# Performance work log

Measured on AMD Instinct MI355X. Metric: run time of the kernel, lower is better.

## Reference

```python
import jax, jax.numpy as jnp
import numpy as np

B, S, D, H = 4, 2048, 1024, 16
DK = D // H

def setup_inputs() -> dict:
    key = jax.random.key(0)
    ks = jax.random.split(key, 8)
    scale = 1.0 / np.sqrt(D)
    return {
        "q": jax.random.normal(ks[0], (B, S, D), jnp.float32),
        "k": jax.random.normal(ks[1], (B, S, D), jnp.float32),
        "v": jax.random.normal(ks[2], (B, S, D), jnp.float32),
        "wq": jax.random.normal(ks[3], (D, D), jnp.float32) * scale,
        "bq": jnp.zeros((D,), jnp.float32),
        "wk": jax.random.normal(ks[4], (D, D), jnp.float32) * scale,
        "bk": jnp.zeros((D,), jnp.float32),
        "wv": jax.random.normal(ks[5], (D, D), jnp.float32) * scale,
        "bv": jnp.zeros((D,), jnp.float32),
        "wo": jax.random.normal(ks[6], (D, D), jnp.float32) * scale,
        "bo": jnp.zeros((D,), jnp.float32),
    }

def reference(q, k, v, wq, bq, wk, bk, wv, bv, wo, bo):
    b, s, _ = q.shape
    # projections; split heads -> [b, h, s, d_k]
    def proj(x, w, bias):
        y = x @ w + bias
        return y.reshape(b, -1, H, DK).transpose(0, 2, 1, 3)
    qh, kh, vh = proj(q, wq, bq), proj(k, wk, bk), proj(v, wv, bv)
    scores = jnp.einsum("bhqd,bhkd->bhqk", qh, kh) / np.sqrt(DK).astype(jnp.float32)
    attn = jax.nn.softmax(scores, axis=-1)  # dropout = identity (eval mode)
    out = jnp.einsum("bhqk,bhkd->bhqd", attn, vh)
    out = out.transpose(0, 2, 1, 3).reshape(b, s, D)
    return out @ wo + bo
```

## Files before the change

kernel.cpp:

```cpp
#include <hip/hip_runtime.h>
#include <hip/hip_bf16.h>

#define B_   4
#define S_   2048
#define D_   1024
#define H_   16
#define DK_  64
#define NTOK 8192

typedef __bf16 bf16_t;
typedef __bf16 bf16x8 __attribute__((ext_vector_type(8)));
typedef __bf16 bf16x4 __attribute__((ext_vector_type(4)));
typedef __bf16 bf16x2 __attribute__((ext_vector_type(2)));
typedef float  f32x4  __attribute__((ext_vector_type(4)));
typedef float  f32x16 __attribute__((ext_vector_type(16)));
typedef unsigned u32x4 __attribute__((ext_vector_type(4)));
typedef int    i32x2  __attribute__((ext_vector_type(2)));

__device__ __forceinline__ void gll16(const void* g, void* l) {
  __builtin_amdgcn_global_load_lds(
      (const __attribute__((address_space(1))) void*)g,
      (__attribute__((address_space(3))) void*)l,
      16, 0, 0);
}

__device__ __forceinline__ f32x4 mfma32(bf16x8 a, bf16x8 b, f32x4 c) {
  return __builtin_amdgcn_mfma_f32_16x16x32_bf16(a, b, c, 0, 0, 0);
}

__device__ __forceinline__ f32x16 mfma32x32(bf16x8 a, bf16x8 b, f32x16 c) {
#if defined(__HIP_DEVICE_COMPILE__)
  return __builtin_amdgcn_mfma_f32_32x32x16_bf16(a, b, c, 0, 0, 0);
#else
  (void)a; (void)b;
  return c;
#endif
}

__device__ __forceinline__ float fast_exp2(float x) {
#if defined(__HIP_DEVICE_COMPILE__) && __has_builtin(__builtin_amdgcn_exp2f)
  return __builtin_amdgcn_exp2f(x);
#else
  return exp2f(x);
#endif
}

__device__ __forceinline__ f32x16 zero16() {
  f32x16 z;
#pragma unroll
  for (int i = 0; i < 16; ++i) z[i] = 0.f;
  return z;
}

__device__ __forceinline__ unsigned pkbf(float lo, float hi) {
  bf16x2 t;
  t[0] = (bf16_t)lo;
  t[1] = (bf16_t)hi;
  return __builtin_bit_cast(unsigned, t);
}

__device__ __forceinline__ void plswap(unsigned &x, unsigned &y) {
#if defined(__HIP_DEVICE_COMPILE__)
  i32x2 r = __builtin_amdgcn_permlane32_swap((int)x, (int)y, false, false);
  x = (unsigned)r[0];
  y = (unsigned)r[1];
#endif
}

__device__ __forceinline__ void build_pa(const f32x16 s, bf16x8 &p0, bf16x8 &p1) {
  unsigned A0 = pkbf(fast_exp2(s[0]),  fast_exp2(s[1]));
  unsigned A1 = pkbf(fast_exp2(s[2]),  fast_exp2(s[3]));
  unsigned B0 = pkbf(fast_exp2(s[4]),  fast_exp2(s[5]));
  unsigned B1 = pkbf(fast_exp2(s[6]),  fast_exp2(s[7]));
  unsigned C0 = pkbf(fast_exp2(s[8]),  fast_exp2(s[9]));
  unsigned C1 = pkbf(fast_exp2(s[10]), fast_exp2(s[11]));
  unsigned D0 = pkbf(fast_exp2(s[12]), fast_exp2(s[13]));
  unsigned D1 = pkbf(fast_exp2(s[14]), fast_exp2(s[15]));
  plswap(A0, B0);
  plswap(A1, B1);
  plswap(C0, D0);
  plswap(C1, D1);
  u32x4 lo = {A0, A1, B0, B1};
  u32x4 hi = {C0, C1, D0, D1};
  p0 = __builtin_bit_cast(bf16x8, lo);
  p1 = __builtin_bit_cast(bf16x8, hi);
}

__global__ __launch_bounds__(256) void tobf16(
    const float* __restrict__ q, const float* __restrict__ k,
    const float* __restrict__ v, bf16_t* __restrict__ o) {
  const float* src = (blockIdx.z == 0) ? q : (blockIdx.z == 1) ? k : v;
  bf16_t* dst = o + (size_t)blockIdx.z * 8388608;
  size_t i = ((size_t)blockIdx.x * 256 + threadIdx.x) * 4;
  float4 x = *(const float4*)&src[i];
  bf16x4 y;
  y[0] = (bf16_t)x.x; y[1] = (bf16_t)x.y;
  y[2] = (bf16_t)x.z; y[3] = (bf16_t)x.w;
  *(bf16x4*)&dst[i] = y;
}

__global__ __launch_bounds__(256) void prep_weights(
    const float* __restrict__ wq, const float* __restrict__ wk,
    const float* __restrict__ wv, const float* __restrict__ wo,
    bf16_t* __restrict__ wtHi) {
  const int z = blockIdx.z;
  const float* W = (z == 0) ? wq : (z == 1) ? wk : (z == 2) ? wv : wo;
  const int k0 = blockIdx.x * 64;
  const int n0 = blockIdx.y * 64;
  const int t = threadIdx.x;
  __shared__ float T[64][65];
#pragma unroll
  for (int rr = 0; rr < 4; ++rr) {
    int row = rr * 16 + (t >> 4);
    int cc = (t & 15) * 4;
    const float4 v = *(const float4*)&W[(size_t)(k0 + row) * D_ + n0 + cc];
    T[row][cc + 0] = v.x; T[row][cc + 1] = v.y;
    T[row][cc + 2] = v.z; T[row][cc + 3] = v.w;
  }
  __syncthreads();
  const int n = t >> 2;
  const int kc = (t & 3) * 16;
  bf16x8 h0, h1;
#pragma unroll
  for (int j = 0; j < 16; ++j) {
    float vv = T[kc + j][n];
    if (j < 8) h0[j] = (bf16_t)vv;
    else       h1[j - 8] = (bf16_t)vv;
  }
  size_t ofs = (size_t)z * 1048576 + (size_t)(n0 + n) * D_ + k0 + kc;
  *(bf16x8*)&wtHi[ofs] = h0; *(bf16x8*)&wtHi[ofs + 8] = h1;
}

__global__ __launch_bounds__(256) void gemm_qkv_bf16(
    const bf16_t* __restrict__ Abf,
    const float* __restrict__ bq, const float* __restrict__ bk,
    const float* __restrict__ bv,
    const bf16_t* __restrict__ wtHi, bf16_t* __restrict__ outQKV) {
  const int z = blockIdx.z;
  const bf16_t* A   = Abf + (size_t)z * 8388608;
  const float* bias = (z == 0) ? bq : (z == 1) ? bk : bv;
  const bf16_t* WHi = wtHi + (size_t)z * 1048576;
  bf16_t* Out = outQKV + (size_t)z * 8388608;

  const int row0 = blockIdx.x * 128;
  const int col0 = blockIdx.y * 128;
  const int t = threadIdx.x;
  const int w = t >> 6, L = t & 63;
  const int m = L & 15, g = L >> 4;

  __shared__ __align__(16) bf16_t As2[128 * 64];
  __shared__ __align__(16) bf16_t Whi_s[128 * 64];

  f32x4 acc[4][4];
#pragma unroll
  for (int i = 0; i < 4; ++i)
#pragma unroll
    for (int j = 0; j < 4; ++j) acc[i][j] = (f32x4){0.f, 0.f, 0.f, 0.f};

  const int aw0 = (w & 1) * 64;
  const int bw0 = (w >> 1) * 64;

  int srow[4], scol[4];
#pragma unroll
  for (int i = 0; i < 4; ++i) {
    int slot = i * 256 + t;
    srow[i] = slot >> 3;
    scol[i] = (slot & 7) ^ (srow[i] & 7);
  }

  for (int kt = 0; kt < 16; ++kt) {
    const int k0 = kt * 64;
#pragma unroll
    for (int i = 0; i < 4; ++i) {
      gll16(&A[(size_t)(row0 + srow[i]) * D_ + k0 + scol[i] * 8],
            &As2[i * 2048 + w * 512]);
      gll16(&WHi[(size_t)(col0 + srow[i]) * D_ + k0 + scol[i] * 8],
            &Whi_s[i * 2048 + w * 512]);
    }
    __syncthreads();

#pragma unroll
    for (int kh = 0; kh < 2; ++kh) {
      bf16x8 af[4], wh[4];
#pragma unroll
      for (int it = 0; it < 4; ++it) {
        int row = aw0 + it * 16 + m;
        int sl = ((kh * 4 + g) ^ (m & 7)) * 8;
        af[it] = *(const bf16x8*)&As2[row * 64 + sl];
      }
#pragma unroll
      for (int jt = 0; jt < 4; ++jt) {
        int n = bw0 + jt * 16 + m;
        int sl = ((kh * 4 + g) ^ (m & 7)) * 8;
        wh[jt] = *(const bf16x8*)&Whi_s[n * 64 + sl];
      }
#pragma unroll
      for (int it = 0; it < 4; ++it)
#pragma unroll
        for (int jt = 0; jt < 4; ++jt)
          acc[it][jt] = mfma32(af[it], wh[jt], acc[it][jt]);
    }
    __syncthreads();
  }
#pragma unroll
  for (int jt = 0; jt < 4; ++jt) {
    int col = col0 + bw0 + jt * 16 + m;
    float bcol = bias[col];
    int h = col >> 6, d = col & 63;
#pragma unroll
    for (int it = 0; it < 4; ++it) {
      if (z != 2) {
#pragma unroll
        for (int r = 0; r < 4; ++r) {
          int row = row0 + aw0 + it * 16 + g * 4 + r;
          int b = row >> 11, s = row & 2047;
          Out[((size_t)((b * H_ + h) * S_ + s)) * DK_ + d] =
              (bf16_t)(acc[it][jt][r] + bcol);
        }
      } else {
        int row = row0 + aw0 + it * 16 + g * 4;
        int b = row >> 11, s = row & 2047;
        bf16x4 p4;
#pragma unroll
        for (int r = 0; r < 4; ++r) p4[r] = (bf16_t)(acc[it][jt][r] + bcol);
        *(bf16x4*)&Out[((size_t)((b * H_ + h) * DK_ + d)) * S_ + s] = p4;
      }
    }
  }
}

__global__ __launch_bounds__(256) void gemm_qkv_f32(
    const float* __restrict__ Aq, const float* __restrict__ Ak,
    const float* __restrict__ Av,
    const float* __restrict__ bq, const float* __restrict__ bk,
    const float* __restrict__ bv,
    const bf16_t* __restrict__ wtHi, bf16_t* __restrict__ outQKV) {
  const int z = blockIdx.z;
  const float* A    = (z == 0) ? Aq : (z == 1) ? Ak : Av;
  const float* bias = (z == 0) ? bq : (z == 1) ? bk : bv;
  const bf16_t* WHi = wtHi + (size_t)z * 1048576;
  bf16_t* Out = outQKV + (size_t)z * 8388608;

  const int row0 = blockIdx.x * 128;
  const int col0 = blockIdx.y * 128;
  const int t = threadIdx.x;
  const int w = t >> 6, L = t & 63;
  const int m = L & 15, g = L >> 4;

  __shared__ __align__(16) float  As[128 * 32];
  __shared__ __align__(16) bf16_t Whi_s[128 * 32];

  f32x4 acc[4][4];
#pragma unroll
  for (int i = 0; i < 4; ++i)
#pragma unroll
    for (int j = 0; j < 4; ++j) acc[i][j] = (f32x4){0.f, 0.f, 0.f, 0.f};

  const int aw0 = (w & 1) * 64;
  const int bw0 = (w >> 1) * 64;

  for (int kt = 0; kt < 32; ++kt) {
    const int k0 = kt * 32;
#pragma unroll
    for (int rr = 0; rr < 4; ++rr) {
      int lin16 = rr * 256 + t;
      int row = lin16 >> 3;
      int c = (lin16 & 7) ^ (row & 7);
      gll16(&A[(size_t)(row0 + row) * D_ + k0 + c * 4], &As[rr * 1024 + w * 256]);
    }
#pragma unroll
    for (int rr = 0; rr < 2; ++rr) {
      int lin16 = rr * 256 + t;
      int n = lin16 >> 2;
      int c = (lin16 & 3) ^ ((n >> 1) & 3);
      gll16(&WHi[(size_t)(col0 + n) * D_ + k0 + c * 8], &Whi_s[rr * 2048 + w * 512]);
    }
    __syncthreads();

    bf16x8 af[4], wh[4];
#pragma unroll
    for (int it = 0; it < 4; ++it) {
      int row = aw0 + it * 16 + m;
      const f32x4* p = (const f32x4*)&As[row * 32];
      f32x4 x0 = p[(2 * g) ^ (m & 7)];
      f32x4 x1 = p[(2 * g + 1) ^ (m & 7)];
      bf16x8 a;
      a[0] = (bf16_t)x0.x; a[1] = (bf16_t)x0.y; a[2] = (bf16_t)x0.z; a[3] = (bf16_t)x0.w;
      a[4] = (bf16_t)x1.x; a[5] = (bf16_t)x1.y; a[6] = (bf16_t)x1.z; a[7] = (bf16_t)x1.w;
      af[it] = a;
    }
#pragma unroll
    for (int jt = 0; jt < 4; ++jt) {
      int n = bw0 + jt * 16 + m;
      int sl = (g ^ ((m >> 1) & 3)) * 8;
      wh[jt] = *(const bf16x8*)&Whi_s[n * 32 + sl];
    }
#pragma unroll
    for (int it = 0; it < 4; ++it)
#pragma unroll
      for (int jt = 0; jt < 4; ++jt)
        acc[it][jt] = mfma32(af[it], wh[jt], acc[it][jt]);
    __syncthreads();
  }
#pragma unroll
  for (int jt = 0; jt < 4; ++jt) {
    int col = col0 + bw0 + jt * 16 + m;
    float bcol = bias[col];
    int h = col >> 6, d = col & 63;
#pragma unroll
    for (int it = 0; it < 4; ++it) {
      if (z != 2) {
#pragma unroll
        for (int r = 0; r < 4; ++r) {
          int row = row0 + aw0 + it * 16 + g * 4 + r;
          int b = row >> 11, s = row & 2047;
          Out[((size_t)((b * H_ + h) * S_ + s)) * DK_ + d] =
              (bf16_t)(acc[it][jt][r] + bcol);
        }
      } else {
        int row = row0 + aw0 + it * 16 + g * 4;
        int b = row >> 11, s = row & 2047;
        bf16x4 p4;
#pragma unroll
        for (int r = 0; r < 4; ++r) p4[r] = (bf16_t)(acc[it][jt][r] + bcol);
        *(bf16x4*)&Out[((size_t)((b * H_ + h) * DK_ + d)) * S_ + s] = p4;
      }
    }
  }
}

__global__ __launch_bounds__(256, 2) void attn(
    const bf16_t* __restrict__ Qh, const bf16_t* __restrict__ Kh,
    const bf16_t* __restrict__ VhT, bf16_t* __restrict__ Ohi) {
  const int bh = blockIdx.y;
  const int q0 = blockIdx.x * 128;
  const int t = threadIdx.x, w = t >> 6;
  const int lane = t & 63;
  const int lo5 = lane & 31, hi = lane >> 5;

  __shared__ __align__(16) bf16_t Ks[64 * 64];
  __shared__ __align__(16) bf16_t Vt[64 * 64];

  const size_t qbase = (size_t)bh * S_ * DK_;
  const size_t vbase = (size_t)bh * DK_ * S_;

  const int qrow = q0 + w * 32 + lo5;
  bf16x8 qf[4];
#pragma unroll
  for (int ks = 0; ks < 4; ++ks) {
    bf16x8 v = *(const bf16x8*)&Qh[qbase + (size_t)qrow * DK_ + ks * 16 + hi * 8];
#pragma unroll
    for (int j = 0; j < 8; ++j) v[j] = (bf16_t)(0.18033688f * (float)v[j]);
    qf[ks] = v;
  }

  bf16x8 ones;
#pragma unroll
  for (int j = 0; j < 8; ++j) ones[j] = (bf16_t)1.f;

  int offs[4];
#pragma unroll
  for (int ks = 0; ks < 4; ++ks)
    offs[ks] = lo5 * 64 + (((ks * 2 + hi) ^ (lo5 & 7)) * 8);

  f32x16 oacc0 = zero16(), oacc1 = zero16(), lacc = zero16();

  for (int kv0 = 0; kv0 < S_; kv0 += 64) {
#pragma unroll
    for (int rr = 0; rr < 2; ++rr) {
      int lin16 = rr * 256 + t;
      int rrow = lin16 >> 3;
      int c = (lin16 & 7) ^ (rrow & 7);
      gll16(&Kh[qbase + (size_t)(kv0 + rrow) * DK_ + c * 8], &Ks[rr * 2048 + w * 512]);
      gll16(&VhT[vbase + (size_t)rrow * S_ + kv0 + c * 8], &Vt[rr * 2048 + w * 512]);
    }
    __syncthreads();

    f32x16 sc0 = zero16(), sc1 = zero16();
#pragma unroll
    for (int ks = 0; ks < 4; ++ks) {
      bf16x8 k0 = *(const bf16x8*)&Ks[offs[ks]];
      bf16x8 k1 = *(const bf16x8*)&Ks[offs[ks] + 2048];
      sc0 = mfma32x32(k0, qf[ks], sc0);
      sc1 = mfma32x32(k1, qf[ks], sc1);
    }

    bf16x8 pa0, pa1, pa2, pa3;
    build_pa(sc0, pa0, pa1);
    build_pa(sc1, pa2, pa3);

#pragma unroll
    for (int ks = 0; ks < 4; ++ks) {
      bf16x8 pb = (ks == 0) ? pa0 : (ks == 1) ? pa1 : (ks == 2) ? pa2 : pa3;
      lacc = mfma32x32(ones, pb, lacc);
      bf16x8 v0 = *(const bf16x8*)&Vt[offs[ks]];
      bf16x8 v1 = *(const bf16x8*)&Vt[offs[ks] + 2048];
      oacc0 = mfma32x32(v0, pb, oacc0);
      oacc1 = mfma32x32(v1, pb, oacc1);
    }
    __syncthreads();
  }

  const int b = bh >> 4, h = bh & 15;
  const float inv = 1.f / lacc[0];
  const size_t rowofs = ((size_t)(b * S_ + qrow)) * D_ + h * DK_;
#pragma unroll
  for (int rg = 0; rg < 4; ++rg) {
    bf16x4 o0, o1;
#pragma unroll
    for (int j = 0; j < 4; ++j) {
      o0[j] = (bf16_t)(oacc0[rg * 4 + j] * inv);
      o1[j] = (bf16_t)(oacc1[rg * 4 + j] * inv);
    }
    *(bf16x4*)&Ohi[rowofs + rg * 8 + hi * 4] = o0;
    *(bf16x4*)&Ohi[rowofs + 32 + rg * 8 + hi * 4] = o1;
  }
}

__global__ __launch_bounds__(256) void gemm_out(
    const bf16_t* __restrict__ Ahi, const bf16_t* __restrict__ wtHi,
    const float* __restrict__ bias, float* __restrict__ Out) {
  const bf16_t* WHi = wtHi + (size_t)3 * 1048576;
  const int row0 = blockIdx.x * 128;
  const int col0 = blockIdx.y * 128;
  const int t = threadIdx.x;
  const int w = t >> 6, L = t & 63;
  const int m = L & 15, g = L >> 4;

  __shared__ __align__(16) bf16_t Ahi_s[128 * 64];
  __shared__ __align__(16) bf16_t Whi_s[128 * 64];

  f32x4 acc[4][4];
#pragma unroll
  for (int i = 0; i < 4; ++i)
#pragma unroll
    for (int j = 0; j < 4; ++j) acc[i][j] = (f32x4){0.f, 0.f, 0.f, 0.f};

  const int aw0 = (w & 1) * 64;
  const int bw0 = (w >> 1) * 64;

  int srow[4], scol[4];
#pragma unroll
  for (int i = 0; i < 4; ++i) {
    int slot = i * 256 + t;
    srow[i] = slot >> 3;
    scol[i] = (slot & 7) ^ (srow[i] & 7);
  }

  for (int kt = 0; kt < 16; ++kt) {
    const int k0 = kt * 64;
#pragma unroll
    for (int i = 0; i < 4; ++i) {
      gll16(&Ahi[(size_t)(row0 + srow[i]) * D_ + k0 + scol[i] * 8],
            &Ahi_s[i * 2048 + w * 512]);
      gll16(&WHi[(size_t)(col0 + srow[i]) * D_ + k0 + scol[i] * 8],
            &Whi_s[i * 2048 + w * 512]);
    }
    __syncthreads();

#pragma unroll
    for (int kh = 0; kh < 2; ++kh) {
      bf16x8 ah[4], wh[4];
#pragma unroll
      for (int it = 0; it < 4; ++it) {
        int row = aw0 + it * 16 + m;
        int sl = ((kh * 4 + g) ^ (m & 7)) * 8;
        ah[it] = *(const bf16x8*)&Ahi_s[row * 64 + sl];
      }
#pragma unroll
      for (int jt = 0; jt < 4; ++jt) {
        int n = bw0 + jt * 16 + m;
        int sl = ((kh * 4 + g) ^ (m & 7)) * 8;
        wh[jt] = *(const bf16x8*)&Whi_s[n * 64 + sl];
      }
#pragma unroll
      for (int it = 0; it < 4; ++it)
#pragma unroll
        for (int jt = 0; jt < 4; ++jt)
          acc[it][jt] = mfma32(ah[it], wh[jt], acc[it][jt]);
    }
    __syncthreads();
  }
#pragma unroll
  for (int jt = 0; jt < 4; ++jt) {
    int col = col0 + bw0 + jt * 16 + m;
    float bcol = bias[col];
#pragma unroll
    for (int it = 0; it < 4; ++it)
#pragma unroll
      for (int r = 0; r < 4; ++r) {
        int row = row0 + aw0 + it * 16 + g * 4 + r;
        Out[(size_t)row * D_ + col] = acc[it][jt][r] + bcol;
      }
  }
}

extern "C" void kernel_launch(void* const* d_in, const int* in_sizes, int n_in,
                              void* d_out, int out_size, void* d_ws, size_t ws_size,
                              hipStream_t stream) {
  const float* q  = (const float*)d_in[0];
  const float* k  = (const float*)d_in[1];
  const float* v  = (const float*)d_in[2];
  const float* wq = (const float*)d_in[3];
  const float* bq = (const float*)d_in[4];
  const float* wk = (const float*)d_in[5];
  const float* bk = (const float*)d_in[6];
  const float* wv = (const float*)d_in[7];
  const float* bv = (const float*)d_in[8];
  const float* wo = (const float*)d_in[9];
  const float* bo = (const float*)d_in[10];
  float* out = (float*)d_out;

  char* ws = (char*)d_ws;
  bf16_t* wtHi = (bf16_t*)(ws);
  bf16_t* QKVh = (bf16_t*)(ws + (8ull << 20));
  bf16_t* Ohi  = (bf16_t*)(ws + (56ull << 20));
  bf16_t* Abf  = (bf16_t*)(ws + (56ull << 20));

  const bool big = ws_size >= (104ull << 20);

  hipLaunchKernelGGL(prep_weights, dim3(16, 16, 4), dim3(256), 0, stream,
                     wq, wk, wv, wo, wtHi);
  if (big) {
    hipLaunchKernelGGL(tobf16, dim3(8192, 1, 3), dim3(256), 0, stream,
                       q, k, v, Abf);
    hipLaunchKernelGGL(gemm_qkv_bf16, dim3(64, 8, 3), dim3(256), 0, stream,
                       Abf, bq, bk, bv, wtHi, QKVh);
  } else {
    hipLaunchKernelGGL(gemm_qkv_f32, dim3(64, 8, 3), dim3(256), 0, stream,
                       q, k, v, bq, bk, bv, wtHi, QKVh);
  }
  hipLaunchKernelGGL(attn, dim3(16, 64), dim3(256), 0, stream,
                     QKVh, QKVh + 8388608, QKVh + 16777216, Ohi);
  hipLaunchKernelGGL(gemm_out, dim3(64, 8), dim3(256), 0, stream,
                     Ohi, wtHi, bo, out);
}
```

Measured before the change: 339.6 us.

## Fuse fp32-to-bf16 input conversion into QKV projection GEMM staging

Drops the separate tobf16 pass and the workspace-size branch. The QKV GEMM now loads fp32 activations into registers, packs them to bf16, and writes them into the same swizzled LDS layout the bf16 GEMM used, with 64-wide K tiles. This removes a full read-convert-write round trip of the activations through global memory and one launch. In exchange, the A-tile load becomes synchronous register loads plus LDS stores instead of async global_load_lds, which may expose load latency, and each A tile is re-read as fp32 by the 8 column blocks.

```diff
diff --git a/kernel.cpp b/kernel.cpp
--- a/kernel.cpp
+++ b/kernel.cpp
@@ -86,19 +86,6 @@
   p1 = __builtin_bit_cast(bf16x8, hi);
 }
 
-__global__ __launch_bounds__(256) void tobf16(
-    const float* __restrict__ q, const float* __restrict__ k,
-    const float* __restrict__ v, bf16_t* __restrict__ o) {
-  const float* src = (blockIdx.z == 0) ? q : (blockIdx.z == 1) ? k : v;
-  bf16_t* dst = o + (size_t)blockIdx.z * 8388608;
-  size_t i = ((size_t)blockIdx.x * 256 + threadIdx.x) * 4;
-  float4 x = *(const float4*)&src[i];
-  bf16x4 y;
-  y[0] = (bf16_t)x.x; y[1] = (bf16_t)x.y;
-  y[2] = (bf16_t)x.z; y[3] = (bf16_t)x.w;
-  *(bf16x4*)&dst[i] = y;
-}
-
 __global__ __launch_bounds__(256) void prep_weights(
     const float* __restrict__ wq, const float* __restrict__ wk,
     const float* __restrict__ wv, const float* __restrict__ wo,
@@ -131,105 +118,7 @@
   *(bf16x8*)&wtHi[ofs] = h0; *(bf16x8*)&wtHi[ofs + 8] = h1;
 }
 
-__global__ __launch_bounds__(256) void gemm_qkv_bf16(
-    const bf16_t* __restrict__ Abf,
-    const float* __restrict__ bq, const float* __restrict__ bk,
-    const float* __restrict__ bv,
-    const bf16_t* __restrict__ wtHi, bf16_t* __restrict__ outQKV) {
-  const int z = blockIdx.z;
-  const bf16_t* A   = Abf + (size_t)z * 8388608;
-  const float* bias = (z == 0) ? bq : (z == 1) ? bk : bv;
-  const bf16_t* WHi = wtHi + (size_t)z * 1048576;
-  bf16_t* Out = outQKV + (size_t)z * 8388608;
-
-  const int row0 = blockIdx.x * 128;
-  const int col0 = blockIdx.y * 128;
-  const int t = threadIdx.x;
-  const int w = t >> 6, L = t & 63;
-  const int m = L & 15, g = L >> 4;
-
-  __shared__ __align__(16) bf16_t As2[128 * 64];
-  __shared__ __align__(16) bf16_t Whi_s[128 * 64];
-
-  f32x4 acc[4][4];
-#pragma unroll
-  for (int i = 0; i < 4; ++i)
-#pragma unroll
-    for (int j = 0; j < 4; ++j) acc[i][j] = (f32x4){0.f, 0.f, 0.f, 0.f};
-
-  const int aw0 = (w & 1) * 64;
-  const int bw0 = (w >> 1) * 64;
-
-  int srow[4], scol[4];
-#pragma unroll
-  for (int i = 0; i < 4; ++i) {
-    int slot = i * 256 + t;
-    srow[i] = slot >> 3;
-    scol[i] = (slot & 7) ^ (srow[i] & 7);
-  }
-
-  for (int kt = 0; kt < 16; ++kt) {
-    const int k0 = kt * 64;
-#pragma unroll
-    for (int i = 0; i < 4; ++i) {
-      gll16(&A[(size_t)(row0 + srow[i]) * D_ + k0 + scol[i] * 8],
-            &As2[i * 2048 + w * 512]);
-      gll16(&WHi[(size_t)(col0 + srow[i]) * D_ + k0 + scol[i] * 8],
-            &Whi_s[i * 2048 + w * 512]);
-    }
-    __syncthreads();
-
-#pragma unroll
-    for (int kh = 0; kh < 2; ++kh) {
-      bf16x8 af[4], wh[4];
-#pragma unroll
-      for (int it = 0; it < 4; ++it) {
-        int row = aw0 + it * 16 + m;
-        int sl = ((kh * 4 + g) ^ (m & 7)) * 8;
-        af[it] = *(const bf16x8*)&As2[row * 64 + sl];
-      }
-#pragma unroll
-      for (int jt = 0; jt < 4; ++jt) {
-        int n = bw0 + jt * 16 + m;
-        int sl = ((kh * 4 + g) ^ (m & 7)) * 8;
-        wh[jt] = *(const bf16x8*)&Whi_s[n * 64 + sl];
-      }
-#pragma unroll
-      for (int it = 0; it < 4; ++it)
-#pragma unroll
-        for (int jt = 0; jt < 4; ++jt)
-          acc[it][jt] = mfma32(af[it], wh[jt], acc[it][jt]);
-    }
-    __syncthreads();
-  }
-#pragma unroll
-  for (int jt = 0; jt < 4; ++jt) {
-    int col = col0 + bw0 + jt * 16 + m;
-    float bcol = bias[col];
-    int h = col >> 6, d = col & 63;
-#pragma unroll
-    for (int it = 0; it < 4; ++it) {
-      if (z != 2) {
-#pragma unroll
-        for (int r = 0; r < 4; ++r) {
-          int row = row0 + aw0 + it * 16 + g * 4 + r;
-          int b = row >> 11, s = row & 2047;
-          Out[((size_t)((b * H_ + h) * S_ + s)) * DK_ + d] =
-              (bf16_t)(acc[it][jt][r] + bcol);
-        }
-      } else {
-        int row = row0 + aw0 + it * 16 + g * 4;
-        int b = row >> 11, s = row & 2047;
-        bf16x4 p4;
-#pragma unroll
-        for (int r = 0; r < 4; ++r) p4[r] = (bf16_t)(acc[it][jt][r] + bcol);
-        *(bf16x4*)&Out[((size_t)((b * H_ + h) * DK_ + d)) * S_ + s] = p4;
-      }
-    }
-  }
-}
-
-__global__ __launch_bounds__(256) void gemm_qkv_f32(
+__global__ __launch_bounds__(256) void gemm_qkv_fused(
     const float* __restrict__ Aq, const float* __restrict__ Ak,
     const float* __restrict__ Av,
     const float* __restrict__ bq, const float* __restrict__ bk,
@@ -247,8 +136,8 @@
   const int w = t >> 6, L = t & 63;
   const int m = L & 15, g = L >> 4;
 
-  __shared__ __align__(16) float  As[128 * 32];
-  __shared__ __align__(16) bf16_t Whi_s[128 * 32];
+  __shared__ __align__(16) bf16_t As2[128 * 64];
+  __shared__ __align__(16) bf16_t Whi_s[128 * 64];
 
   f32x4 acc[4][4];
 #pragma unroll
@@ -259,47 +148,53 @@
   const int aw0 = (w & 1) * 64;
   const int bw0 = (w >> 1) * 64;
 
-  for (int kt = 0; kt < 32; ++kt) {
-    const int k0 = kt * 32;
-#pragma unroll
-    for (int rr = 0; rr < 4; ++rr) {
-      int lin16 = rr * 256 + t;
-      int row = lin16 >> 3;
-      int c = (lin16 & 7) ^ (row & 7);
-      gll16(&A[(size_t)(row0 + row) * D_ + k0 + c * 4], &As[rr * 1024 + w * 256]);
-    }
-#pragma unroll
-    for (int rr = 0; rr < 2; ++rr) {
-      int lin16 = rr * 256 + t;
-      int n = lin16 >> 2;
-      int c = (lin16 & 3) ^ ((n >> 1) & 3);
-      gll16(&WHi[(size_t)(col0 + n) * D_ + k0 + c * 8], &Whi_s[rr * 2048 + w * 512]);
-    }
-    __syncthreads();
-
-    bf16x8 af[4], wh[4];
-#pragma unroll
-    for (int it = 0; it < 4; ++it) {
-      int row = aw0 + it * 16 + m;
-      const f32x4* p = (const f32x4*)&As[row * 32];
-      f32x4 x0 = p[(2 * g) ^ (m & 7)];
-      f32x4 x1 = p[(2 * g + 1) ^ (m & 7)];
-      bf16x8 a;
-      a[0] = (bf16_t)x0.x; a[1] = (bf16_t)x0.y; a[2] = (bf16_t)x0.z; a[3] = (bf16_t)x0.w;
-      a[4] = (bf16_t)x1.x; a[5] = (bf16_t)x1.y; a[6] = (bf16_t)x1.z; a[7] = (bf16_t)x1.w;
-      af[it] = a;
-    }
-#pragma unroll
-    for (int jt = 0; jt < 4; ++jt) {
-      int n = bw0 + jt * 16 + m;
-      int sl = (g ^ ((m >> 1) & 3)) * 8;
-      wh[jt] = *(const bf16x8*)&Whi_s[n * 32 + sl];
-    }
-#pragma unroll
-    for (int it = 0; it < 4; ++it)
-#pragma unroll
-      for (int jt = 0; jt < 4; ++jt)
-        acc[it][jt] = mfma32(af[it], wh[jt], acc[it][jt]);
+  int srow[4], scol[4];
+#pragma unroll
+  for (int i = 0; i < 4; ++i) {
+    int slot = i * 256 + t;
+    srow[i] = slot >> 3;
+    scol[i] = (slot & 7) ^ (srow[i] & 7);
+  }
+
+  for (int kt = 0; kt < 16; ++kt) {
+    const int k0 = kt * 64;
+#pragma unroll
+    for (int i = 0; i < 4; ++i) {
+      const float* src = &A[(size_t)(row0 + srow[i]) * D_ + k0 + scol[i] * 8];
+      f32x4 x0 = *(const f32x4*)src;
+      f32x4 x1 = *(const f32x4*)(src + 4);
+      u32x4 pk = {pkbf(x0[0], x0[1]), pkbf(x0[2], x0[3]),
+                  pkbf(x1[0], x1[1]), pkbf(x1[2], x1[3])};
+      *(u32x4*)&As2[(i * 256 + t) * 8] = pk;
+    }
+#pragma unroll
+    for (int i = 0; i < 4; ++i) {
+      gll16(&WHi[(size_t)(col0 + srow[i]) * D_ + k0 + scol[i] * 8],
+            &Whi_s[i * 2048 + w * 512]);
+    }
+    __syncthreads();
+
+#pragma unroll
+    for (int kh = 0; kh < 2; ++kh) {
+      bf16x8 af[4], wh[4];
+#pragma unroll
+      for (int it = 0; it < 4; ++it) {
+        int row = aw0 + it * 16 + m;
+        int sl = ((kh * 4 + g) ^ (m & 7)) * 8;
+        af[it] = *(const bf16x8*)&As2[row * 64 + sl];
+      }
+#pragma unroll
+      for (int jt = 0; jt < 4; ++jt) {
+        int n = bw0 + jt * 16 + m;
+        int sl = ((kh * 4 + g) ^ (m & 7)) * 8;
+        wh[jt] = *(const bf16x8*)&Whi_s[n * 64 + sl];
+      }
+#pragma unroll
+      for (int it = 0; it < 4; ++it)
+#pragma unroll
+        for (int jt = 0; jt < 4; ++jt)
+          acc[it][jt] = mfma32(af[it], wh[jt], acc[it][jt]);
+    }
     __syncthreads();
   }
 #pragma unroll
@@ -515,21 +410,11 @@
   bf16_t* wtHi = (bf16_t*)(ws);
   bf16_t* QKVh = (bf16_t*)(ws + (8ull << 20));
   bf16_t* Ohi  = (bf16_t*)(ws + (56ull << 20));
-  bf16_t* Abf  = (bf16_t*)(ws + (56ull << 20));
-
-  const bool big = ws_size >= (104ull << 20);
 
   hipLaunchKernelGGL(prep_weights, dim3(16, 16, 4), dim3(256), 0, stream,
                      wq, wk, wv, wo, wtHi);
-  if (big) {
-    hipLaunchKernelGGL(tobf16, dim3(8192, 1, 3), dim3(256), 0, stream,
-                       q, k, v, Abf);
-    hipLaunchKernelGGL(gemm_qkv_bf16, dim3(64, 8, 3), dim3(256), 0, stream,
-                       Abf, bq, bk, bv, wtHi, QKVh);
-  } else {
-    hipLaunchKernelGGL(gemm_qkv_f32, dim3(64, 8, 3), dim3(256), 0, stream,
-                       q, k, v, bq, bk, bv, wtHi, QKVh);
-  }
+  hipLaunchKernelGGL(gemm_qkv_fused, dim3(64, 8, 3), dim3(256), 0, stream,
+                     q, k, v, bq, bk, bv, wtHi, QKVh);
   hipLaunchKernelGGL(attn, dim3(16, 64), dim3(256), 0, stream,
                      QKVh, QKVh + 8388608, QKVh + 16777216, Ohi);
   hipLaunchKernelGGL(gemm_out, dim3(64, 8), dim3(256), 0, stream,
```

Result: slower. 354.1 us (+4.3%).

## Merge weight and activation prep kernels; double-buffer output GEMM LDS loads

Applied to the files above, without the earlier changes.

Folds the weight transpose/convert and the activation fp32-to-bf16 conversion into one launch, which removes one kernel launch and lets the two jobs run concurrently. The output projection GEMM now keeps two LDS buffers and issues the next K-tile's global-to-LDS loads before computing on the current tile, so load latency overlaps the MFMA work. This doubles the GEMM's LDS footprint, which may reduce occupancy.

```diff
diff --git a/kernel.cpp b/kernel.cpp
--- a/kernel.cpp
+++ b/kernel.cpp
@@ -86,49 +86,54 @@
   p1 = __builtin_bit_cast(bf16x8, hi);
 }
 
-__global__ __launch_bounds__(256) void tobf16(
+__global__ __launch_bounds__(256) void prep_all(
     const float* __restrict__ q, const float* __restrict__ k,
-    const float* __restrict__ v, bf16_t* __restrict__ o) {
-  const float* src = (blockIdx.z == 0) ? q : (blockIdx.z == 1) ? k : v;
-  bf16_t* dst = o + (size_t)blockIdx.z * 8388608;
-  size_t i = ((size_t)blockIdx.x * 256 + threadIdx.x) * 4;
-  float4 x = *(const float4*)&src[i];
-  bf16x4 y;
-  y[0] = (bf16_t)x.x; y[1] = (bf16_t)x.y;
-  y[2] = (bf16_t)x.z; y[3] = (bf16_t)x.w;
-  *(bf16x4*)&dst[i] = y;
-}
-
-__global__ __launch_bounds__(256) void prep_weights(
+    const float* __restrict__ v,
     const float* __restrict__ wq, const float* __restrict__ wk,
     const float* __restrict__ wv, const float* __restrict__ wo,
-    bf16_t* __restrict__ wtHi) {
-  const int z = blockIdx.z;
-  const float* W = (z == 0) ? wq : (z == 1) ? wk : (z == 2) ? wv : wo;
-  const int k0 = blockIdx.x * 64;
-  const int n0 = blockIdx.y * 64;
+    bf16_t* __restrict__ wtHi, bf16_t* __restrict__ Abf) {
+  const int b = blockIdx.x;
   const int t = threadIdx.x;
   __shared__ float T[64][65];
-#pragma unroll
-  for (int rr = 0; rr < 4; ++rr) {
-    int row = rr * 16 + (t >> 4);
-    int cc = (t & 15) * 4;
-    const float4 v = *(const float4*)&W[(size_t)(k0 + row) * D_ + n0 + cc];
-    T[row][cc + 0] = v.x; T[row][cc + 1] = v.y;
-    T[row][cc + 2] = v.z; T[row][cc + 3] = v.w;
-  }
-  __syncthreads();
-  const int n = t >> 2;
-  const int kc = (t & 3) * 16;
-  bf16x8 h0, h1;
-#pragma unroll
-  for (int j = 0; j < 16; ++j) {
-    float vv = T[kc + j][n];
-    if (j < 8) h0[j] = (bf16_t)vv;
-    else       h1[j - 8] = (bf16_t)vv;
-  }
-  size_t ofs = (size_t)z * 1048576 + (size_t)(n0 + n) * D_ + k0 + kc;
-  *(bf16x8*)&wtHi[ofs] = h0; *(bf16x8*)&wtHi[ofs + 8] = h1;
+
+  if (b < 1024) {
+    const int z = b >> 8;
+    const float* W = (z == 0) ? wq : (z == 1) ? wk : (z == 2) ? wv : wo;
+    const int k0 = (b & 15) * 64;
+    const int n0 = ((b >> 4) & 15) * 64;
+#pragma unroll
+    for (int rr = 0; rr < 4; ++rr) {
+      int row = rr * 16 + (t >> 4);
+      int cc = (t & 15) * 4;
+      const float4 vv = *(const float4*)&W[(size_t)(k0 + row) * D_ + n0 + cc];
+      T[row][cc + 0] = vv.x; T[row][cc + 1] = vv.y;
+      T[row][cc + 2] = vv.z; T[row][cc + 3] = vv.w;
+    }
+    __syncthreads();
+    const int n = t >> 2;
+    const int kc = (t & 3) * 16;
+    bf16x8 h0, h1;
+#pragma unroll
+    for (int j = 0; j < 16; ++j) {
+      float vv = T[kc + j][n];
+      if (j < 8) h0[j] = (bf16_t)vv;
+      else       h1[j - 8] = (bf16_t)vv;
+    }
+    size_t ofs = (size_t)z * 1048576 + (size_t)(n0 + n) * D_ + k0 + kc;
+    *(bf16x8*)&wtHi[ofs] = h0; *(bf16x8*)&wtHi[ofs + 8] = h1;
+  } else {
+    const int bb = b - 1024;
+    const int z = bb >> 13;
+    const int xb = bb & 8191;
+    const float* src = (z == 0) ? q : (z == 1) ? k : v;
+    bf16_t* dst = Abf + (size_t)z * 8388608;
+    size_t i = ((size_t)xb * 256 + t) * 4;
+    float4 x = *(const float4*)&src[i];
+    bf16x4 y;
+    y[0] = (bf16_t)x.x; y[1] = (bf16_t)x.y;
+    y[2] = (bf16_t)x.z; y[3] = (bf16_t)x.w;
+    *(bf16x4*)&dst[i] = y;
+  }
 }
 
 __global__ __launch_bounds__(256) void gemm_qkv_bf16(
@@ -427,8 +432,8 @@
   const int w = t >> 6, L = t & 63;
   const int m = L & 15, g = L >> 4;
 
-  __shared__ __align__(16) bf16_t Ahi_s[128 * 64];
-  __shared__ __align__(16) bf16_t Whi_s[128 * 64];
+  __shared__ __align__(16) bf16_t Ahi_s[2][128 * 64];
+  __shared__ __align__(16) bf16_t Whi_s[2][128 * 64];
 
   f32x4 acc[4][4];
 #pragma unroll
@@ -447,17 +452,26 @@
     scol[i] = (slot & 7) ^ (srow[i] & 7);
   }
 
+#define OSTAGE(buf, k0)                                                        \
+  do {                                                                         \
+    _Pragma("unroll")                                                          \
+    for (int i = 0; i < 4; ++i) {                                              \
+      gll16(&Ahi[(size_t)(row0 + srow[i]) * D_ + (k0) + scol[i] * 8],          \
+            &Ahi_s[buf][i * 2048 + w * 512]);                                  \
+      gll16(&WHi[(size_t)(col0 + srow[i]) * D_ + (k0) + scol[i] * 8],          \
+            &Whi_s[buf][i * 2048 + w * 512]);                                  \
+    }                                                                          \
+  } while (0)
+
+  OSTAGE(0, 0);
+  __syncthreads();
+
   for (int kt = 0; kt < 16; ++kt) {
-    const int k0 = kt * 64;
-#pragma unroll
-    for (int i = 0; i < 4; ++i) {
-      gll16(&Ahi[(size_t)(row0 + srow[i]) * D_ + k0 + scol[i] * 8],
-            &Ahi_s[i * 2048 + w * 512]);
-      gll16(&WHi[(size_t)(col0 + srow[i]) * D_ + k0 + scol[i] * 8],
-            &Whi_s[i * 2048 + w * 512]);
-    }
-    __syncthreads();
-
+    const int c = kt & 1;
+    if (kt < 15) OSTAGE(c ^ 1, (kt + 1) * 64);
+
+    const bf16_t* as_b = &Ahi_s[c][0];
+    const bf16_t* ws_b = &Whi_s[c][0];
 #pragma unroll
     for (int kh = 0; kh < 2; ++kh) {
       bf16x8 ah[4], wh[4];
@@ -465,13 +479,13 @@
       for (int it = 0; it < 4; ++it) {
         int row = aw0 + it * 16 + m;
         int sl = ((kh * 4 + g) ^ (m & 7)) * 8;
-        ah[it] = *(const bf16x8*)&Ahi_s[row * 64 + sl];
+        ah[it] = *(const bf16x8*)&as_b[row * 64 + sl];
       }
 #pragma unroll
       for (int jt = 0; jt < 4; ++jt) {
         int n = bw0 + jt * 16 + m;
         int sl = ((kh * 4 + g) ^ (m & 7)) * 8;
-        wh[jt] = *(const bf16x8*)&Whi_s[n * 64 + sl];
+        wh[jt] = *(const bf16x8*)&ws_b[n * 64 + sl];
       }
 #pragma unroll
       for (int it = 0; it < 4; ++it)
@@ -481,6 +495,8 @@
     }
     __syncthreads();
   }
+#undef OSTAGE
+
 #pragma unroll
   for (int jt = 0; jt < 4; ++jt) {
     int col = col0 + bw0 + jt * 16 + m;
@@ -519,14 +535,14 @@
 
   const bool big = ws_size >= (104ull << 20);
 
-  hipLaunchKernelGGL(prep_weights, dim3(16, 16, 4), dim3(256), 0, stream,
-                     wq, wk, wv, wo, wtHi);
   if (big) {
-    hipLaunchKernelGGL(tobf16, dim3(8192, 1, 3), dim3(256), 0, stream,
-                       q, k, v, Abf);
+    hipLaunchKernelGGL(prep_all, dim3(25600), dim3(256), 0, stream,
+                       q, k, v, wq, wk, wv, wo, wtHi, Abf);
     hipLaunchKernelGGL(gemm_qkv_bf16, dim3(64, 8, 3), dim3(256), 0, stream,
                        Abf, bq, bk, bv, wtHi, QKVh);
   } else {
+    hipLaunchKernelGGL(prep_all, dim3(1024), dim3(256), 0, stream,
+                       q, k, v, wq, wk, wv, wo, wtHi, (bf16_t*)wtHi );
     hipLaunchKernelGGL(gemm_qkv_f32, dim3(64, 8, 3), dim3(256), 0, stream,
                        q, k, v, bq, bk, bv, wtHi, QKVh);
   }
```

Result: no change. 339.7 us (+0.0%).
